# Optimization experiments

Measured on AMD Instinct MI355X. Metric: run time of the kernel, lower is better.

Reference implementation:

```python
import jax, jax.numpy as jnp
import numpy as np

N_HEADS = 8  # init n_heads

def setup_inputs() -> dict:
    key = jax.random.key(0)
    ks = jax.random.split(key, 5)
    hid = 128  # = init hidden_dim // 2
    h = jax.random.normal(ks[0], (4, 4097, hid), dtype=jnp.float32)  # n=4096 nodes + 1 aux node
    init = lambda k, shp, fan: jax.random.normal(k, shp, dtype=jnp.float32) / np.float32(np.sqrt(fan))
    W_q = init(ks[1], (hid, hid), hid)        # stored (in, out); torch Linear applies x @ W.T
    W_kv = init(ks[2], (hid, 2 * hid), hid)
    W_mhc = init(ks[3], (hid, hid), hid)
    W_lin = init(ks[4], (2, 1), 2)            # (2, edge_out_dim)
    return {"h": h, "W_q": W_q, "W_kv": W_kv, "W_mhc": W_mhc, "W_lin": W_lin}

def reference(h, W_q, W_kv, W_mhc, W_lin):
    # aux_node=True: last row is the graph embedding h_g
    hn, hg = h[:, :-1, :], h[:, -1:, :]
    bp, n, hid = hn.shape
    D = hid // N_HEADS  # head_dim
    # single-query multi-head attention: q from aux node, k/v from nodes
    q = (hg @ W_q).reshape(bp, 1, N_HEADS, D).transpose(0, 2, 1, 3)       # (bp,H,1,D)
    kv = hn @ W_kv
    k = kv[..., :hid].reshape(bp, n, N_HEADS, D).transpose(0, 2, 1, 3)    # (bp,H,n,D)
    v = kv[..., hid:].reshape(bp, n, N_HEADS, D).transpose(0, 2, 1, 3)    # (bp,H,n,D)
    scale = 1.0 / jnp.sqrt(jnp.float32(D))
    attn = jax.nn.softmax(jnp.einsum('bhqd,bhkd->bhqk', q, k) * scale, axis=-1)
    y = jnp.einsum('bhqk,bhkd->bhqd', attn, v)                            # (bp,H,1,D)
    y = y.transpose(0, 2, 1, 3).reshape(bp, 1, hid)
    mh = y @ W_mhc                                                        # (bp,1,hid)
    # per-node scalar score: y2[b,i] = <mh[b], hn[b,i]>
    y2 = jnp.einsum('boh,bnh->bn', mh, hn)                                # (bp,n)
    # pairwise edge features [y_j, y_i] -> linear(2->edge_out_dim), fused as
    # e[b,i,j,o] = y2[b,j]*W_lin[0,o] + y2[b,i]*W_lin[1,o]
    e = y2[:, None, :, None] * W_lin[0] + y2[:, :, None, None] * W_lin[1]  # (bp,n,n,E)
    return e.reshape(bp, n * n, W_lin.shape[1])
```

## Files before the change

### kernel.cpp

```cpp
#include <hip/hip_runtime.h>
#include <math.h>

#define HID 128
#define NH  8
#define DH  16
#define NN  4096
#define BP  4
#define SEQ 4097

#define WS_T   0
#define WS_L   4096
#define WS_A   4128
#define WS_B   (WS_A + BP * NN)

#define UPAD 132

typedef float f32x4 __attribute__((ext_vector_type(4)));

__global__ void k1_score_acc(const float* __restrict__ h,
                             const float* __restrict__ W_q,
                             const float* __restrict__ W_kv,
                             float* __restrict__ ws) {
    __shared__ float hg_sh[HID];
    __shared__ float q_sh[HID];
    __shared__ float u_sh[NH * UPAD];
    __shared__ float p_sh[256];
    __shared__ float red[256];
    const int blk = blockIdx.x;
    const int b = blk >> 7;
    const int j0 = (blk & 127) * 32;
    const int t = threadIdx.x;
    const float* hb = h + (size_t)b * SEQ * HID;

    if (t < HID) hg_sh[t] = hb[(size_t)NN * HID + t];
    __syncthreads();
    if (t < HID) {
        float a = 0.f;
        #pragma unroll 8
        for (int c = 0; c < HID; ++c) a = fmaf(hg_sh[c], W_q[c * HID + t], a);
        q_sh[t] = a;
    }
    __syncthreads();
    for (int i = t; i < NH * HID; i += 256) {
        const int hh = i >> 7, c = i & 127;
        float a = 0.f;
        #pragma unroll
        for (int d = 0; d < DH; ++d)
            a = fmaf(W_kv[c * 2 * HID + hh * DH + d], q_sh[hh * DH + d], a);
        u_sh[hh * UPAD + c] = a * 0.25f;
    }
    __syncthreads();

    const int hh = t & 7;
    const int jl = t >> 3;
    const float4* hrow = (const float4*)(hb + (size_t)(j0 + jl) * HID);
    const float4* uu = (const float4*)(u_sh + hh * UPAD);
    float acc = 0.f;
    #pragma unroll
    for (int c4 = 0; c4 < HID / 4; ++c4) {
        float4 hv = hrow[c4];
        float4 uv = uu[c4];
        acc = fmaf(hv.x, uv.x, acc);
        acc = fmaf(hv.y, uv.y, acc);
        acc = fmaf(hv.z, uv.z, acc);
        acc = fmaf(hv.w, uv.w, acc);
    }
    const float p = __expf(acc);
    p_sh[t] = p;
    red[t] = p;
    __syncthreads();
    #pragma unroll
    for (int off = 128; off >= 8; off >>= 1) {
        if (t < off) red[t] += red[t + off];
        __syncthreads();
    }
    if (t < 8) atomicAdd(ws + WS_L + b * NH + t, red[t]);

    const int c = t & 127;
    const int jh = t >> 7;
    float acc2[NH];
    #pragma unroll
    for (int k = 0; k < NH; ++k) acc2[k] = 0.f;
    for (int j = jh; j < 32; j += 2) {
        float hv = hb[(size_t)(j0 + j) * HID + c];
        #pragma unroll
        for (int k = 0; k < NH; ++k)
            acc2[k] = fmaf(p_sh[j * 8 + k], hv, acc2[k]);
    }
    float* tb = ws + WS_T + (size_t)b * NH * HID;
    #pragma unroll
    for (int k = 0; k < NH; ++k)
        atomicAdd(tb + k * HID + c, acc2[k]);
}

__global__ void kE_y2(const float* __restrict__ h,
                      const float* __restrict__ W_kv,
                      const float* __restrict__ W_mhc,
                      const float* __restrict__ W_lin,
                      float* __restrict__ ws) {
    __shared__ float y_sh[HID];
    __shared__ float mh_sh[HID];
    const int blk = blockIdx.x;
    const int b = blk >> 5;
    const int t = threadIdx.x;
    const int j = (blk & 31) * 128 + t;

    const float* tb = ws + WS_T + (size_t)b * NH * HID;
    const int hh = t >> 4;
    float a = 0.f;
    #pragma unroll 8
    for (int c = 0; c < HID; ++c)
        a = fmaf(tb[hh * HID + c], W_kv[c * 2 * HID + HID + t], a);
    y_sh[t] = a / ws[WS_L + b * NH + hh];
    __syncthreads();
    float mo = 0.f;
    #pragma unroll 8
    for (int hd = 0; hd < HID; ++hd)
        mo = fmaf(y_sh[hd], W_mhc[hd * HID + t], mo);
    mh_sh[t] = mo;
    __syncthreads();

    const float4* hrow = (const float4*)(h + (size_t)b * SEQ * HID + (size_t)j * HID);
    const float4* mm = (const float4*)mh_sh;
    float acc = 0.f;
    #pragma unroll
    for (int c4 = 0; c4 < HID / 4; ++c4) {
        float4 hv = hrow[c4];
        float4 mv = mm[c4];
        acc = fmaf(hv.x, mv.x, acc);
        acc = fmaf(hv.y, mv.y, acc);
        acc = fmaf(hv.z, mv.z, acc);
        acc = fmaf(hv.w, mv.w, acc);
    }
    ws[WS_A + (size_t)b * NN + j] = W_lin[0] * acc;
    ws[WS_B + (size_t)b * NN + j] = W_lin[1] * acc;
}

__global__ void kF_emit(const float* __restrict__ ws,
                        float* __restrict__ out) {
    const int blk = blockIdx.x;
    const int b = blk >> 12;
    const int i = blk & (NN - 1);
    const float add = ws[WS_B + (size_t)b * NN + i];
    const f32x4* arow = (const f32x4*)(ws + WS_A + (size_t)b * NN);
    f32x4* orow = (f32x4*)(out + ((size_t)b << 24) + ((size_t)i << 12));
    #pragma unroll
    for (int k = threadIdx.x; k < NN / 4; k += 256) {
        f32x4 v = arow[k] + add;
        __builtin_nontemporal_store(v, orow + k);
    }
}

extern "C" void kernel_launch(void* const* d_in, const int* in_sizes, int n_in,
                              void* d_out, int out_size, void* d_ws, size_t ws_size,
                              hipStream_t stream) {
    const float* h     = (const float*)d_in[0];
    const float* W_q   = (const float*)d_in[1];
    const float* W_kv  = (const float*)d_in[2];
    const float* W_mhc = (const float*)d_in[3];
    const float* W_lin = (const float*)d_in[4];
    float* out = (float*)d_out;
    float* ws = (float*)d_ws;

    hipMemsetAsync(ws + WS_T, 0, (4096 + 32) * sizeof(float), stream);

    k1_score_acc<<<BP * 128, 256, 0, stream>>>(h, W_q, W_kv, ws);
    kE_y2<<<BP * 32, 128, 0, stream>>>(h, W_kv, W_mhc, W_lin, ws);
    kF_emit<<<BP * NN, 256, 0, stream>>>(ws, out);
}
```

Measured before the change: 322.6 us.

## Hoist q/u projection into a prep kernel, use shuffle reduction, plain stores

Moves the per-batch q and u=W_k·q projection out of each of the 512 score blocks into a small prep kernel that also zeroes the accumulators, replacing the hipMemsetAsync. The score kernel now reads u from global memory and reduces exp sums with wave shuffles instead of a shared-memory tree with many barriers. The emit kernel switches from nontemporal stores to regular stores. The redundant projection work goes away, but the change adds a kernel launch and a serial dependency. The output write dominates runtime, so the store change matters most and could help or hurt.

```diff
diff --git a/kernel.cpp b/kernel.cpp
--- a/kernel.cpp
+++ b/kernel.cpp
@@ -12,25 +12,22 @@
 #define WS_L   4096
 #define WS_A   4128
 #define WS_B   (WS_A + BP * NN)
-
-#define UPAD 132
+#define WS_U   (WS_B + BP * NN)
 
 typedef float f32x4 __attribute__((ext_vector_type(4)));
 
-__global__ void k1_score_acc(const float* __restrict__ h,
-                             const float* __restrict__ W_q,
-                             const float* __restrict__ W_kv,
-                             float* __restrict__ ws) {
+__global__ void k0_prep(const float* __restrict__ h,
+                        const float* __restrict__ W_q,
+                        const float* __restrict__ W_kv,
+                        float* __restrict__ ws) {
     __shared__ float hg_sh[HID];
     __shared__ float q_sh[HID];
-    __shared__ float u_sh[NH * UPAD];
-    __shared__ float p_sh[256];
-    __shared__ float red[256];
-    const int blk = blockIdx.x;
-    const int b = blk >> 7;
-    const int j0 = (blk & 127) * 32;
+    const int b = blockIdx.x;
     const int t = threadIdx.x;
     const float* hb = h + (size_t)b * SEQ * HID;
+
+    for (int i = t; i < NH * HID; i += 256) ws[WS_T + b * NH * HID + i] = 0.f;
+    if (t < NH) ws[WS_L + b * NH + t] = 0.f;
 
     if (t < HID) hg_sh[t] = hb[(size_t)NN * HID + t];
     __syncthreads();
@@ -47,14 +44,24 @@
         #pragma unroll
         for (int d = 0; d < DH; ++d)
             a = fmaf(W_kv[c * 2 * HID + hh * DH + d], q_sh[hh * DH + d], a);
-        u_sh[hh * UPAD + c] = a * 0.25f;
+        ws[WS_U + b * NH * HID + i] = a * 0.25f;
     }
-    __syncthreads();
+}
+
+__global__ void k1_score_acc(const float* __restrict__ h,
+                             float* __restrict__ ws) {
+    __shared__ float p_sh[256];
+    __shared__ float redw[4 * NH];
+    const int blk = blockIdx.x;
+    const int b = blk >> 7;
+    const int j0 = (blk & 127) * 32;
+    const int t = threadIdx.x;
+    const float* hb = h + (size_t)b * SEQ * HID;
 
     const int hh = t & 7;
     const int jl = t >> 3;
     const float4* hrow = (const float4*)(hb + (size_t)(j0 + jl) * HID);
-    const float4* uu = (const float4*)(u_sh + hh * UPAD);
+    const float4* uu = (const float4*)(ws + WS_U + ((size_t)b * NH + hh) * HID);
     float acc = 0.f;
     #pragma unroll
     for (int c4 = 0; c4 < HID / 4; ++c4) {
@@ -67,14 +74,17 @@
     }
     const float p = __expf(acc);
     p_sh[t] = p;
-    red[t] = p;
+
+    float psum = p;
+    psum += __shfl_xor(psum, 8);
+    psum += __shfl_xor(psum, 16);
+    psum += __shfl_xor(psum, 32);
+    const int wid = t >> 6, lane = t & 63;
+    if (lane < NH) redw[wid * NH + lane] = psum;
     __syncthreads();
-    #pragma unroll
-    for (int off = 128; off >= 8; off >>= 1) {
-        if (t < off) red[t] += red[t + off];
-        __syncthreads();
-    }
-    if (t < 8) atomicAdd(ws + WS_L + b * NH + t, red[t]);
+    if (t < NH)
+        atomicAdd(ws + WS_L + b * NH + t,
+                  redw[t] + redw[NH + t] + redw[2 * NH + t] + redw[3 * NH + t]);
 
     const int c = t & 127;
     const int jh = t >> 7;
@@ -147,7 +157,7 @@
     #pragma unroll
     for (int k = threadIdx.x; k < NN / 4; k += 256) {
         f32x4 v = arow[k] + add;
-        __builtin_nontemporal_store(v, orow + k);
+        orow[k] = v;
     }
 }
 
@@ -162,9 +172,8 @@
     float* out = (float*)d_out;
     float* ws = (float*)d_ws;
 
-    hipMemsetAsync(ws + WS_T, 0, (4096 + 32) * sizeof(float), stream);
-
-    k1_score_acc<<<BP * 128, 256, 0, stream>>>(h, W_q, W_kv, ws);
+    k0_prep<<<BP, 256, 0, stream>>>(h, W_q, W_kv, ws);
+    k1_score_acc<<<BP * 128, 256, 0, stream>>>(h, ws);
     kE_y2<<<BP * 32, 128, 0, stream>>>(h, W_kv, W_mhc, W_lin, ws);
     kF_emit<<<BP * NN, 256, 0, stream>>>(ws, out);
 }
```

Measured after the change: 329.4 us. 1.02x slower.
